# Performance work log

Hardware: AMD Instinct MI355X
Metric: run time of the kernel (lower is better)

The kernel has to match this reference:

```python
import jax, jax.numpy as jnp
import numpy as np

DIM = 256
H_GLOBAL = 8
H_LOCAL = 4  # max(1, num_heads // 2)
WINDOW = 5
HALF = WINDOW // 2
B, S = 4, 2048
EPS = 1e-5


def layer_norm(x, g, b):
    mu = jnp.mean(x, axis=-1, keepdims=True)
    var = jnp.mean(jnp.square(x - mu), axis=-1, keepdims=True)
    return (x - mu) * jax.lax.rsqrt(var + EPS) * g + b


def qkv_proj(x, in_w, in_b):
    qkv = x @ in_w.T + in_b
    return jnp.split(qkv, 3, axis=-1)


def global_mha(x, in_w, in_b, out_w, out_b, nh):
    Bq, Sq, D = x.shape
    hd = D // nh
    q, k, v = qkv_proj(x, in_w, in_b)
    q = q.reshape(Bq, Sq, nh, hd)
    k = k.reshape(Bq, Sq, nh, hd)
    v = v.reshape(Bq, Sq, nh, hd)
    scores = jnp.einsum('bqhd,bkhd->bhqk', q, k) / np.sqrt(hd).astype(np.float32)
    attn = jax.nn.softmax(scores, axis=-1)
    o = jnp.einsum('bhqk,bkhd->bqhd', attn, v).reshape(Bq, Sq, D)
    return o @ out_w.T + out_b


def local_mha(x, in_w, in_b, out_w, out_b, nh):
    # banded sliding-window attention, window = 2*HALF+1, per-query softmax
    Bq, Sq, D = x.shape
    hd = D // nh
    q, k, v = qkv_proj(x, in_w, in_b)
    kp = jnp.pad(k, ((0, 0), (HALF, HALF), (0, 0)))
    vp = jnp.pad(v, ((0, 0), (HALF, HALF), (0, 0)))
    # [B, S, W, D] windows of keys/values around each query position
    k_win = jnp.stack([kp[:, j:j + Sq] for j in range(WINDOW)], axis=2)
    v_win = jnp.stack([vp[:, j:j + Sq] for j in range(WINDOW)], axis=2)
    q = q.reshape(Bq, Sq, nh, hd)
    k_win = k_win.reshape(Bq, Sq, WINDOW, nh, hd)
    v_win = v_win.reshape(Bq, Sq, WINDOW, nh, hd)
    scores = jnp.einsum('bshd,bswhd->bshw', q, k_win) / np.sqrt(hd).astype(np.float32)
    idx = jnp.arange(Sq)[:, None] + jnp.arange(-HALF, HALF + 1)[None, :]  # [S, W]
    valid = (idx >= 0) & (idx < Sq)
    scores = jnp.where(valid[None, :, None, :], scores, -jnp.inf)
    attn = jax.nn.softmax(scores, axis=-1)
    o = jnp.einsum('bshw,bswhd->bshd', attn, v_win).reshape(Bq, Sq, D)
    return o @ out_w.T + out_b


def setup_inputs() -> dict:
    key = jax.random.key(0)
    ks = jax.random.split(key, 8)
    sc = 0.02
    d = DIM
    return {
        'x': jax.random.normal(ks[0], (B, S, d), jnp.float32),
        'g_in_w': jax.random.normal(ks[1], (3 * d, d), jnp.float32) * sc,
        'g_in_b': jnp.zeros((3 * d,), jnp.float32),
        'g_out_w': jax.random.normal(ks[2], (d, d), jnp.float32) * sc,
        'g_out_b': jnp.zeros((d,), jnp.float32),
        't_in_w': jax.random.normal(ks[3], (3 * d, d), jnp.float32) * sc,
        't_in_b': jnp.zeros((3 * d,), jnp.float32),
        't_out_w': jax.random.normal(ks[4], (d, d), jnp.float32) * sc,
        't_out_b': jnp.zeros((d,), jnp.float32),
        'fus_w1': jax.random.normal(ks[5], (2 * d, 2 * d), jnp.float32) * sc,
        'fus_b1': jnp.zeros((2 * d,), jnp.float32),
        'fus_w2': jax.random.normal(ks[6], (d, 2 * d), jnp.float32) * sc,
        'fus_b2': jnp.zeros((d,), jnp.float32),
        'ffn_w1': jax.random.normal(ks[7], (2 * d, d), jnp.float32) * sc,
        'ffn_b1': jnp.zeros((2 * d,), jnp.float32),
        'ffn_w2': jax.random.normal(jax.random.fold_in(key, 9), (d, 2 * d), jnp.float32) * sc,
        'ffn_b2': jnp.zeros((d,), jnp.float32),
        'gn_g': jnp.ones((d,), jnp.float32),
        'gn_b': jnp.zeros((d,), jnp.float32),
        'fn_g': jnp.ones((d,), jnp.float32),
        'fn_b': jnp.zeros((d,), jnp.float32),
    }


def reference(x, g_in_w, g_in_b, g_out_w, g_out_b,
              t_in_w, t_in_b, t_out_w, t_out_b,
              fus_w1, fus_b1, fus_w2, fus_b2,
              ffn_w1, ffn_b1, ffn_w2, ffn_b2,
              gn_g, gn_b, fn_g, fn_b):
    x_global = global_mha(x, g_in_w, g_in_b, g_out_w, g_out_b, H_GLOBAL)
    x_local = local_mha(x, t_in_w, t_in_b, t_out_w, t_out_b, H_LOCAL)
    x_comb = jnp.concatenate([x_global, x_local], axis=-1)
    x_fused = jax.nn.silu(x_comb @ fus_w1.T + fus_b1) @ fus_w2.T + fus_b2
    x = layer_norm(x + x_fused, gn_g, gn_b)
    x_ffn = jax.nn.silu(x @ ffn_w1.T + ffn_b1) @ ffn_w2.T + ffn_b2
    x = layer_norm(x + x_ffn, fn_g, fn_b)
    return x
```

## Files before the change

### kernel.cpp

```cpp
#include <hip/hip_runtime.h>

constexpr int Bb = 4;
constexpr int Ss = 2048;
constexpr int QSTR = 1536;

typedef __bf16 bf16x8 __attribute__((ext_vector_type(8)));
typedef __bf16 bf16x4 __attribute__((ext_vector_type(4)));
typedef float  f32x4  __attribute__((ext_vector_type(4)));

__device__ __forceinline__ void glds16(const void* g, void* l) {
    __builtin_amdgcn_global_load_lds(
        (const __attribute__((address_space(1))) unsigned int*)g,
        (__attribute__((address_space(3))) unsigned int*)l, 16, 0, 0);
}

struct CvtArgs {
    const float* src[9];
    __bf16* dst[9];
    int start[10];
};

__global__ __launch_bounds__(256) void convert_all(CvtArgs a)
{
    int e = 0;
    const int bid = blockIdx.x;
#pragma unroll
    for (int i = 0; i < 8; i++) if (bid >= a.start[i + 1]) e = i + 1;
    const int idx = (bid - a.start[e]) * 256 + threadIdx.x;
    const float* s = a.src[e];
    float4 v0 = *(const float4*)&s[(size_t)idx * 8];
    float4 v1 = *(const float4*)&s[(size_t)idx * 8 + 4];
    bf16x8 o;
    o[0] = (__bf16)v0.x; o[1] = (__bf16)v0.y; o[2] = (__bf16)v0.z; o[3] = (__bf16)v0.w;
    o[4] = (__bf16)v1.x; o[5] = (__bf16)v1.y; o[6] = (__bf16)v1.z; o[7] = (__bf16)v1.w;
    *(bf16x8*)&a.dst[e][(size_t)idx * 8] = o;
}

__global__ __launch_bounds__(256) void gemm128(
    const __bf16* __restrict__ A, const __bf16* __restrict__ W,
    const float* __restrict__ bias, const float* __restrict__ bias2, int bsplit,
    __bf16* __restrict__ C, int K, int ldc)
{
    __shared__ __bf16 As[128 * 64];
    __shared__ __bf16 Ws[128 * 64];
    const int tid = threadIdx.x;
    const int lane = tid & 63;
    const int wv = tid >> 6;
    const int wm = (wv >> 1) * 64;
    const int wn = (wv & 1) * 64;
    const int qrow = lane & 15;
    const int quad = lane >> 4;
    const int n0 = blockIdx.x * 128;
    const int m0 = blockIdx.y * 128;

    f32x4 acc[4][4];
#pragma unroll
    for (int i = 0; i < 4; i++)
#pragma unroll
        for (int j = 0; j < 4; j++) acc[i][j] = {0.f, 0.f, 0.f, 0.f};

    for (int k0 = 0; k0 < K; k0 += 64) {
        __syncthreads();
#pragma unroll
        for (int i = 0; i < 4; i++) {
            const int c = (wv * 4 + i) * 64 + lane;
            const int row = c >> 3, g = c & 7;
            const int gs = (g ^ (row & 7)) * 8;
            glds16(&A[(size_t)(m0 + row) * K + k0 + gs], &As[(wv * 4 + i) * 512]);
            glds16(&W[(size_t)(n0 + row) * K + k0 + gs], &Ws[(wv * 4 + i) * 512]);
        }
        __syncthreads();
#pragma unroll
        for (int ksub = 0; ksub < 2; ksub++) {
            const int gl = ksub * 4 + quad;
            bf16x8 af[4], bf[4];
#pragma unroll
            for (int mi = 0; mi < 4; mi++) {
                const int row = wm + mi * 16 + qrow;
                af[mi] = *(const bf16x8*)&As[row * 64 + (gl ^ (row & 7)) * 8];
            }
#pragma unroll
            for (int ni = 0; ni < 4; ni++) {
                const int row = wn + ni * 16 + qrow;
                bf[ni] = *(const bf16x8*)&Ws[row * 64 + (gl ^ (row & 7)) * 8];
            }
#pragma unroll
            for (int mi = 0; mi < 4; mi++)
#pragma unroll
                for (int ni = 0; ni < 4; ni++)
                    acc[mi][ni] = __builtin_amdgcn_mfma_f32_16x16x32_bf16(
                        af[mi], bf[ni], acc[mi][ni], 0, 0, 0);
        }
    }

    float bz[4];
#pragma unroll
    for (int ni = 0; ni < 4; ni++) {
        const int n = n0 + wn + ni * 16 + qrow;
        bz[ni] = (n < bsplit) ? bias[n] : bias2[n - bsplit];
    }
#pragma unroll
    for (int mi = 0; mi < 4; mi++)
#pragma unroll
        for (int r = 0; r < 4; r++) {
            const int row = m0 + wm + mi * 16 + quad * 4 + r;
#pragma unroll
            for (int ni = 0; ni < 4; ni++) {
                float v = acc[mi][ni][r] + bz[ni];
                C[(size_t)row * ldc + n0 + wn + ni * 16 + qrow] = (__bf16)v;
            }
        }
}

template<bool SILU, bool OUT_BF16>
__global__ __launch_bounds__(256) void gemm_small(
    const __bf16* __restrict__ A0, const __bf16* __restrict__ W0,
    const float* __restrict__ bias0, const __bf16* __restrict__ W1,
    const float* __restrict__ bias1, int nsplit, int aoff1, int coff1,
    void* __restrict__ C, int lda, int K, int ldc)
{
    __shared__ __bf16 As[32 * 128];
    __shared__ __bf16 Ws[64 * 128];
    const int tid = threadIdx.x;
    const int lane = tid & 63;
    const int wv = tid >> 6;
    const int wm = (wv >> 1) * 16;
    const int wn = (wv & 1) * 32;
    const int qrow = lane & 15;
    const int quad = lane >> 4;
    const bool second = (int)blockIdx.x >= nsplit;
    const int bx = second ? (blockIdx.x - nsplit) : blockIdx.x;
    const __bf16* A = second ? (A0 + aoff1) : A0;
    const __bf16* W = second ? W1 : W0;
    const float* bias = second ? bias1 : bias0;
    const int coff = second ? coff1 : 0;
    const int n0 = bx * 64;
    const int m0 = blockIdx.y * 32;

    f32x4 acc[2];
    acc[0] = {0.f, 0.f, 0.f, 0.f};
    acc[1] = {0.f, 0.f, 0.f, 0.f};

    for (int k0 = 0; k0 < K; k0 += 128) {
        __syncthreads();
#pragma unroll
        for (int i = 0; i < 2; i++) {
            const int c = (wv * 2 + i) * 64 + lane;
            const int row = c >> 4, s = c & 15;
            const int gs = ((s & 8) | ((s ^ row) & 7)) * 8;
            glds16(&A[(size_t)(m0 + row) * lda + k0 + gs], &As[(wv * 2 + i) * 512]);
        }
#pragma unroll
        for (int i = 0; i < 4; i++) {
            const int c = (wv * 4 + i) * 64 + lane;
            const int row = c >> 4, s = c & 15;
            const int gs = ((s & 8) | ((s ^ row) & 7)) * 8;
            glds16(&W[(size_t)(n0 + row) * K + k0 + gs], &Ws[(wv * 4 + i) * 512]);
        }
        __syncthreads();
#pragma unroll
        for (int ksub = 0; ksub < 4; ksub++) {
            const int gl = ksub * 4 + quad;
            bf16x8 af, bf[2];
            {
                const int row = wm + qrow;
                const int s = (gl & 8) | ((gl ^ row) & 7);
                af = *(const bf16x8*)&As[row * 128 + s * 8];
            }
#pragma unroll
            for (int ni = 0; ni < 2; ni++) {
                const int row = wn + ni * 16 + qrow;
                const int s = (gl & 8) | ((gl ^ row) & 7);
                bf[ni] = *(const bf16x8*)&Ws[row * 128 + s * 8];
            }
#pragma unroll
            for (int ni = 0; ni < 2; ni++)
                acc[ni] = __builtin_amdgcn_mfma_f32_16x16x32_bf16(
                    af, bf[ni], acc[ni], 0, 0, 0);
        }
    }

    float bz[2];
#pragma unroll
    for (int ni = 0; ni < 2; ni++) bz[ni] = bias[n0 + wn + ni * 16 + qrow];

#pragma unroll
    for (int r = 0; r < 4; r++) {
        const int row = m0 + wm + quad * 4 + r;
#pragma unroll
        for (int ni = 0; ni < 2; ni++) {
            float v = acc[ni][r] + bz[ni];
            if (SILU) v = v / (1.f + __expf(-v));
            const int col = coff + n0 + wn + ni * 16 + qrow;
            if (OUT_BF16)
                ((__bf16*)C)[(size_t)row * ldc + col] = (__bf16)v;
            else
                ((float*)C)[(size_t)row * ldc + col] = v;
        }
    }
}

__global__ __launch_bounds__(512) void attn_fused(
    const __bf16* __restrict__ qkv, __bf16* __restrict__ Op,
    float* __restrict__ Lp, __bf16* __restrict__ acat)
{
    __shared__ __bf16 Kl[64 * 32];
    __shared__ __bf16 Vt[32 * 72];
    __shared__ __bf16 Pl[8][16 * 72];

    const int t = threadIdx.x;
    const int lane = t & 63;
    const int wv = t >> 6;

    if (blockIdx.x < 2048) {
        const int bid = blockIdx.x;
        const int sp = bid & 3;
        const int qc = (bid >> 2) & 15;
        const int h  = (bid >> 6) & 7;
        const int b  = bid >> 9;
        const int bS = b * Ss;
        const int q0 = qc * 128;

        const int qrow = lane & 15;
        const int quad = lane >> 4;
        const float cQ = 1.4426950408889634f * 0.17677669529663687f;

        bf16x8 qf;
        {
            bf16x8 qraw = *(const bf16x8*)(qkv +
                (size_t)(bS + q0 + wv * 16 + qrow) * QSTR + h * 32 + quad * 8);
#pragma unroll
            for (int i = 0; i < 8; i++) qf[i] = (__bf16)((float)qraw[i] * cQ);
        }
        bf16x8 ones;
#pragma unroll
        for (int i = 0; i < 8; i++) ones[i] = (__bf16)1.0f;

        f32x4 o0 = {0.f, 0.f, 0.f, 0.f};
        f32x4 o1 = {0.f, 0.f, 0.f, 0.f};
        f32x4 lac = {0.f, 0.f, 0.f, 0.f};
        const f32x4 z = {0.f, 0.f, 0.f, 0.f};

        const int kc_c = wv * 64 + lane;
        const int kkey = kc_c >> 2, kdg = kc_c & 3;
        const int vkey = t & 63, vq = t >> 6;

        for (int kc = sp * 8; kc < sp * 8 + 8; kc++) {
            __syncthreads();
            if (wv < 4)
                glds16(qkv + (size_t)(bS + kc * 64 + kkey) * QSTR + 256 + h * 32 + kdg * 8,
                       &Kl[wv * 512]);
            {
                const __bf16* src = qkv + (size_t)(bS + kc * 64 + vkey) * QSTR
                                    + 512 + h * 32 + vq * 4;
                bf16x4 v = *(const bf16x4*)src;
#pragma unroll
                for (int i = 0; i < 4; i++) Vt[(vq * 4 + i) * 72 + vkey] = v[i];
            }
            __syncthreads();

            f32x4 s[4];
#pragma unroll
            for (int kg = 0; kg < 4; kg++) {
                bf16x8 kf = *(const bf16x8*)&Kl[(kg * 16 + qrow) * 32 + quad * 8];
                s[kg] = __builtin_amdgcn_mfma_f32_16x16x32_bf16(kf, qf, z, 0, 0, 0);
            }
#pragma unroll
            for (int kg = 0; kg < 4; kg++) {
                bf16x4 pk;
                pk[0] = (__bf16)exp2f(s[kg][0]);
                pk[1] = (__bf16)exp2f(s[kg][1]);
                pk[2] = (__bf16)exp2f(s[kg][2]);
                pk[3] = (__bf16)exp2f(s[kg][3]);
                *(bf16x4*)&Pl[wv][qrow * 72 + kg * 16 + quad * 4] = pk;
            }
            bf16x8 pf0 = *(const bf16x8*)&Pl[wv][qrow * 72 + quad * 8];
            bf16x8 pf1 = *(const bf16x8*)&Pl[wv][qrow * 72 + 32 + quad * 8];
            bf16x8 vf00 = *(const bf16x8*)&Vt[qrow * 72 + quad * 8];
            bf16x8 vf01 = *(const bf16x8*)&Vt[qrow * 72 + 32 + quad * 8];
            bf16x8 vf10 = *(const bf16x8*)&Vt[(16 + qrow) * 72 + quad * 8];
            bf16x8 vf11 = *(const bf16x8*)&Vt[(16 + qrow) * 72 + 32 + quad * 8];
            o0 = __builtin_amdgcn_mfma_f32_16x16x32_bf16(vf00, pf0, o0, 0, 0, 0);
            o1 = __builtin_amdgcn_mfma_f32_16x16x32_bf16(vf10, pf0, o1, 0, 0, 0);
            lac = __builtin_amdgcn_mfma_f32_16x16x32_bf16(ones, pf0, lac, 0, 0, 0);
            o0 = __builtin_amdgcn_mfma_f32_16x16x32_bf16(vf01, pf1, o0, 0, 0, 0);
            o1 = __builtin_amdgcn_mfma_f32_16x16x32_bf16(vf11, pf1, o1, 0, 0, 0);
            lac = __builtin_amdgcn_mfma_f32_16x16x32_bf16(ones, pf1, lac, 0, 0, 0);
        }

        const int gid = (b * 8 + h) * 2048 + q0 + wv * 16 + qrow;
        __bf16* po = Op + (size_t)sp * 2097152 + (size_t)gid * 32;
        bf16x4 w0, w1;
#pragma unroll
        for (int r = 0; r < 4; r++) { w0[r] = (__bf16)o0[r]; w1[r] = (__bf16)o1[r]; }
        *(bf16x4*)&po[quad * 4]      = w0;
        *(bf16x4*)&po[16 + quad * 4] = w1;
        if (quad == 0) Lp[sp * 65536 + gid] = lac[0];
    } else {
        const int w = (blockIdx.x - 2048) * 8 + wv;
        const int b = w >> 13;
        const int rem = w & 8191;
        const int s = rem >> 2;
        const int h = rem & 3;

        const float q = (float)qkv[(size_t)(b * Ss + s) * QSTR + 768 + h * 64 + lane];
        float sc[5], vv[5];
#pragma unroll
        for (int j = 0; j < 5; j++) {
            int pos = s + j - 2;
            bool valid = (pos >= 0) && (pos < Ss);
            int cpos = valid ? pos : 0;
            const size_t rb = (size_t)(b * Ss + cpos) * QSTR;
            float kj = valid ? (float)qkv[rb + 1024 + h * 64 + lane] : 0.f;
            vv[j] = valid ? (float)qkv[rb + 1280 + h * 64 + lane] : 0.f;
            float p = q * kj;
#pragma unroll
            for (int off = 32; off > 0; off >>= 1) p += __shfl_xor(p, off, 64);
            sc[j] = valid ? p * 0.125f : -1e30f;
        }
        float m = sc[0];
#pragma unroll
        for (int j = 1; j < 5; j++) m = fmaxf(m, sc[j]);
        float l = 0.f, o = 0.f;
#pragma unroll
        for (int j = 0; j < 5; j++) {
            float p = __expf(sc[j] - m);
            l += p; o += p * vv[j];
        }
        acat[(size_t)(b * Ss + s) * 512 + 256 + h * 64 + lane] = (__bf16)(o / l);
    }
}

__global__ __launch_bounds__(256) void attn_combine(
    const __bf16* __restrict__ Op, const float* __restrict__ Lp,
    __bf16* __restrict__ acat)
{
    const int t = blockIdx.x * 256 + threadIdx.x;
    const int gid = t >> 3;
    const int dg = t & 7;
    const int b = gid >> 14;
    const int h = (gid >> 11) & 7;
    const int q = gid & 2047;

    const float li = 1.f / (Lp[gid] + Lp[65536 + gid] + Lp[131072 + gid] + Lp[196608 + gid]);
    const __bf16* base = Op + (size_t)gid * 32 + dg * 4;
    bf16x4 a0 = *(const bf16x4*)&base[0];
    bf16x4 a1 = *(const bf16x4*)&base[2097152];
    bf16x4 a2 = *(const bf16x4*)&base[4194304];
    bf16x4 a3 = *(const bf16x4*)&base[6291456];
    bf16x4 r;
#pragma unroll
    for (int i = 0; i < 4; i++)
        r[i] = (__bf16)(((float)a0[i] + (float)a1[i] + (float)a2[i] + (float)a3[i]) * li);
    *(bf16x4*)&acat[(size_t)(b * Ss + q) * 512 + h * 32 + dg * 4] = r;
}

__global__ __launch_bounds__(256) void ln_residual(
    const float* __restrict__ a, const __bf16* __restrict__ r,
    const float* __restrict__ g, const float* __restrict__ be,
    float* __restrict__ out, __bf16* __restrict__ ob)
{
    const int lane = threadIdx.x & 63;
    const int tok = blockIdx.x * 4 + (threadIdx.x >> 6);
    float4 xa = ((const float4*)a)[(size_t)tok * 64 + lane];
    bf16x4 xr = *(const bf16x4*)&r[(size_t)tok * 256 + lane * 4];
    float4 x;
    x.x = xa.x + (float)xr[0]; x.y = xa.y + (float)xr[1];
    x.z = xa.z + (float)xr[2]; x.w = xa.w + (float)xr[3];
    float sum = x.x + x.y + x.z + x.w;
#pragma unroll
    for (int off = 32; off > 0; off >>= 1) sum += __shfl_xor(sum, off, 64);
    float mu = sum * (1.f / 256.f);
    float4 c;
    c.x = x.x - mu; c.y = x.y - mu; c.z = x.z - mu; c.w = x.w - mu;
    float sq = c.x * c.x + c.y * c.y + c.z * c.z + c.w * c.w;
#pragma unroll
    for (int off = 32; off > 0; off >>= 1) sq += __shfl_xor(sq, off, 64);
    float rs = rsqrtf(sq * (1.f / 256.f) + 1e-5f);
    float4 gg = ((const float4*)g)[lane];
    float4 bb = ((const float4*)be)[lane];
    float4 o;
    o.x = c.x * rs * gg.x + bb.x; o.y = c.y * rs * gg.y + bb.y;
    o.z = c.z * rs * gg.z + bb.z; o.w = c.w * rs * gg.w + bb.w;
    ((float4*)out)[(size_t)tok * 64 + lane] = o;
    if (ob) {
        bf16x4 hh;
        hh[0] = (__bf16)o.x; hh[1] = (__bf16)o.y; hh[2] = (__bf16)o.z; hh[3] = (__bf16)o.w;
        *(bf16x4*)&ob[(size_t)tok * 256 + lane * 4] = hh;
    }
}

extern "C" void kernel_launch(void* const* d_in, const int* in_sizes, int n_in,
                              void* d_out, int out_size, void* d_ws, size_t ws_size,
                              hipStream_t stream)
{
    const float* x      = (const float*)d_in[0];
    const float* g_in_w = (const float*)d_in[1];
    const float* g_in_b = (const float*)d_in[2];
    const float* g_out_w= (const float*)d_in[3];
    const float* g_out_b= (const float*)d_in[4];
    const float* t_in_w = (const float*)d_in[5];
    const float* t_in_b = (const float*)d_in[6];
    const float* t_out_w= (const float*)d_in[7];
    const float* t_out_b= (const float*)d_in[8];
    const float* fus_w1 = (const float*)d_in[9];
    const float* fus_b1 = (const float*)d_in[10];
    const float* fus_w2 = (const float*)d_in[11];
    const float* fus_b2 = (const float*)d_in[12];
    const float* ffn_w1 = (const float*)d_in[13];
    const float* ffn_b1 = (const float*)d_in[14];
    const float* ffn_w2 = (const float*)d_in[15];
    const float* ffn_b2 = (const float*)d_in[16];
    const float* gn_g   = (const float*)d_in[17];
    const float* gn_b   = (const float*)d_in[18];
    const float* fn_g   = (const float*)d_in[19];
    const float* fn_b   = (const float*)d_in[20];
    float* out = (float*)d_out;
    float* ws  = (float*)d_ws;

    __bf16* xb     = (__bf16*)(ws);
    __bf16* wb     = (__bf16*)(ws + 1048576);
    __bf16* qkvgl  = (__bf16*)(ws + 1638400);
    __bf16* acat   = (__bf16*)(ws + 7929856);
    __bf16* fcomb  = (__bf16*)(ws + 10027008);
    __bf16* h1     = (__bf16*)(ws + 12124160);
    __bf16* xfb    = (__bf16*)(ws + 14221312);
    float*  x2     = ws + 16318464;
    __bf16* x2b    = (__bf16*)(ws + 18415616);
    __bf16* h2     = h1;
    __bf16* xffb   = xfb;
    __bf16* Op = (__bf16*)(ws + 10027008);
    float*  Lp = ws + 18415616;

    __bf16* w_gin  = wb;
    __bf16* w_gout = wb + 393216;
    __bf16* w_tout = wb + 458752;
    __bf16* w_f1   = wb + 524288;
    __bf16* w_f2   = wb + 786432;
    __bf16* w_n1   = wb + 917504;
    __bf16* w_n2   = wb + 1048576;

    CvtArgs ca;
    ca.src[0] = x;      ca.dst[0] = xb;
    ca.src[1] = g_in_w; ca.dst[1] = w_gin;
    ca.src[2] = t_in_w; ca.dst[2] = w_gin + 196608;
    ca.src[3] = g_out_w;ca.dst[3] = w_gout;
    ca.src[4] = t_out_w;ca.dst[4] = w_tout;
    ca.src[5] = fus_w1; ca.dst[5] = w_f1;
    ca.src[6] = fus_w2; ca.dst[6] = w_f2;
    ca.src[7] = ffn_w1; ca.dst[7] = w_n1;
    ca.src[8] = ffn_w2; ca.dst[8] = w_n2;
    int st[10] = {0, 1024, 1120, 1216, 1248, 1280, 1408, 1472, 1536, 1600};
    for (int i = 0; i < 10; i++) ca.start[i] = st[i];

    convert_all<<<dim3(1600), 256, 0, stream>>>(ca);

    gemm128<<<dim3(12, 64), 256, 0, stream>>>(
        xb, w_gin, g_in_b, t_in_b, 768, qkvgl, 256, QSTR);
    attn_fused<<<dim3(6144), 512, 0, stream>>>(qkvgl, Op, Lp, acat);
    attn_combine<<<dim3(2048), 256, 0, stream>>>(Op, Lp, acat);
    gemm_small<false, true><<<dim3(8, 256), 256, 0, stream>>>(
        acat, w_gout, g_out_b, w_tout, t_out_b, 4, 256, 256, fcomb, 512, 256, 512);
    gemm_small<true,  true><<<dim3(8, 256), 256, 0, stream>>>(
        fcomb, w_f1, fus_b1, w_f1, fus_b1, 1 << 30, 0, 0, h1, 512, 512, 512);
    gemm_small<false, true><<<dim3(4, 256), 256, 0, stream>>>(
        h1, w_f2, fus_b2, w_f2, fus_b2, 1 << 30, 0, 0, xfb, 512, 512, 256);
    ln_residual<<<dim3(2048), 256, 0, stream>>>(x, xfb, gn_g, gn_b, x2, x2b);
    gemm_small<true,  true><<<dim3(8, 256), 256, 0, stream>>>(
        x2b, w_n1, ffn_b1, w_n1, ffn_b1, 1 << 30, 0, 0, h2, 256, 256, 512);
    gemm_small<false, true><<<dim3(4, 256), 256, 0, stream>>>(
        h2, w_n2, ffn_b2, w_n2, ffn_b2, 1 << 30, 0, 0, xffb, 512, 512, 256);
    ln_residual<<<dim3(2048), 256, 0, stream>>>(x2, xffb, fn_g, fn_b, out, nullptr);
}
```

Before: 238.3 us.

## Fuse output GEMM with residual add and LayerNorm into one kernel

Adds a gemm_ln kernel in which each block computes a 32-row by full 256-column output tile, adds bias and the fp32 residual, and does the LayerNorm reduction across waves through shared memory. It replaces the two gemm_small + ln_residual pairs, so two launches go away and the bf16 intermediate is never written to or read back from global memory. The new grid has only 256 blocks, each loading the whole 256xK weight slice per k-step, so parallelism is lower and weight traffic is redundant across blocks. Variance is now computed as E[x^2]-mu^2 and the pre-norm sum stays in fp32 instead of passing through bf16, which slightly changes numerics.

```diff
diff --git a/kernel.cpp b/kernel.cpp
--- a/kernel.cpp
+++ b/kernel.cpp
@@ -200,6 +200,127 @@
     }
 }
 
+__global__ __launch_bounds__(256) void gemm_ln(
+    const __bf16* __restrict__ A, const __bf16* __restrict__ W,
+    const float* __restrict__ bias, const float* __restrict__ xres,
+    const float* __restrict__ g, const float* __restrict__ be,
+    float* __restrict__ out, __bf16* __restrict__ ob, int K)
+{
+    __shared__ __bf16 As[32 * 64];
+    __shared__ __bf16 Ws[256 * 64];
+    __shared__ float redS[4][32];
+    __shared__ float redQ[4][32];
+
+    const int tid = threadIdx.x;
+    const int lane = tid & 63;
+    const int wv = tid >> 6;
+    const int qrow = lane & 15;
+    const int quad = lane >> 4;
+    const int m0 = blockIdx.x * 32;
+
+    f32x4 acc[2][4];
+#pragma unroll
+    for (int mi = 0; mi < 2; mi++)
+#pragma unroll
+        for (int ni = 0; ni < 4; ni++) acc[mi][ni] = {0.f, 0.f, 0.f, 0.f};
+
+    for (int k0 = 0; k0 < K; k0 += 64) {
+        __syncthreads();
+        {
+            const int c = wv * 64 + lane;
+            const int row = c >> 3, gch = c & 7;
+            const int gs = (gch ^ (row & 7)) * 8;
+            glds16(&A[(size_t)(m0 + row) * K + k0 + gs], &As[wv * 512]);
+        }
+#pragma unroll
+        for (int i = 0; i < 8; i++) {
+            const int c = (wv * 8 + i) * 64 + lane;
+            const int row = c >> 3, gch = c & 7;
+            const int gs = (gch ^ (row & 7)) * 8;
+            glds16(&W[(size_t)row * K + k0 + gs], &Ws[(wv * 8 + i) * 512]);
+        }
+        __syncthreads();
+#pragma unroll
+        for (int ksub = 0; ksub < 2; ksub++) {
+            const int gl = ksub * 4 + quad;
+            bf16x8 af[2], bf[4];
+#pragma unroll
+            for (int mi = 0; mi < 2; mi++) {
+                const int row = mi * 16 + qrow;
+                af[mi] = *(const bf16x8*)&As[row * 64 + (gl ^ (row & 7)) * 8];
+            }
+#pragma unroll
+            for (int ni = 0; ni < 4; ni++) {
+                const int row = wv * 64 + ni * 16 + qrow;
+                bf[ni] = *(const bf16x8*)&Ws[row * 64 + (gl ^ (row & 7)) * 8];
+            }
+#pragma unroll
+            for (int mi = 0; mi < 2; mi++)
+#pragma unroll
+                for (int ni = 0; ni < 4; ni++)
+                    acc[mi][ni] = __builtin_amdgcn_mfma_f32_16x16x32_bf16(
+                        af[mi], bf[ni], acc[mi][ni], 0, 0, 0);
+        }
+    }
+
+    float bz[4];
+#pragma unroll
+    for (int ni = 0; ni < 4; ni++) bz[ni] = bias[wv * 64 + ni * 16 + qrow];
+
+#pragma unroll
+    for (int mi = 0; mi < 2; mi++) {
+#pragma unroll
+        for (int r = 0; r < 4; r++) {
+            const int row = m0 + mi * 16 + quad * 4 + r;
+            float s = 0.f, q = 0.f;
+#pragma unroll
+            for (int ni = 0; ni < 4; ni++) {
+                const int col = wv * 64 + ni * 16 + qrow;
+                float v = acc[mi][ni][r] + bz[ni] + xres[(size_t)row * 256 + col];
+                acc[mi][ni][r] = v;
+                s += v; q += v * v;
+            }
+#pragma unroll
+            for (int off = 1; off < 16; off <<= 1) {
+                s += __shfl_xor(s, off, 64);
+                q += __shfl_xor(q, off, 64);
+            }
+            if (qrow == 0) {
+                redS[wv][mi * 16 + quad * 4 + r] = s;
+                redQ[wv][mi * 16 + quad * 4 + r] = q;
+            }
+        }
+    }
+    __syncthreads();
+
+    float gg[4], bb[4];
+#pragma unroll
+    for (int ni = 0; ni < 4; ni++) {
+        const int col = wv * 64 + ni * 16 + qrow;
+        gg[ni] = g[col]; bb[ni] = be[col];
+    }
+#pragma unroll
+    for (int mi = 0; mi < 2; mi++) {
+#pragma unroll
+        for (int r = 0; r < 4; r++) {
+            const int rl = mi * 16 + quad * 4 + r;
+            const float S = redS[0][rl] + redS[1][rl] + redS[2][rl] + redS[3][rl];
+            const float Q = redQ[0][rl] + redQ[1][rl] + redQ[2][rl] + redQ[3][rl];
+            const float mu = S * (1.f / 256.f);
+            const float var = Q * (1.f / 256.f) - mu * mu;
+            const float rs = rsqrtf(var + 1e-5f);
+            const int row = m0 + rl;
+#pragma unroll
+            for (int ni = 0; ni < 4; ni++) {
+                const int col = wv * 64 + ni * 16 + qrow;
+                const float v = (acc[mi][ni][r] - mu) * rs * gg[ni] + bb[ni];
+                out[(size_t)row * 256 + col] = v;
+                if (ob) ob[(size_t)row * 256 + col] = (__bf16)v;
+            }
+        }
+    }
+}
+
 __global__ __launch_bounds__(512) void attn_fused(
     const __bf16* __restrict__ qkv, __bf16* __restrict__ Op,
     float* __restrict__ Lp, __bf16* __restrict__ acat)
@@ -353,41 +474,6 @@
     for (int i = 0; i < 4; i++)
         r[i] = (__bf16)(((float)a0[i] + (float)a1[i] + (float)a2[i] + (float)a3[i]) * li);
     *(bf16x4*)&acat[(size_t)(b * Ss + q) * 512 + h * 32 + dg * 4] = r;
-}
-
-__global__ __launch_bounds__(256) void ln_residual(
-    const float* __restrict__ a, const __bf16* __restrict__ r,
-    const float* __restrict__ g, const float* __restrict__ be,
-    float* __restrict__ out, __bf16* __restrict__ ob)
-{
-    const int lane = threadIdx.x & 63;
-    const int tok = blockIdx.x * 4 + (threadIdx.x >> 6);
-    float4 xa = ((const float4*)a)[(size_t)tok * 64 + lane];
-    bf16x4 xr = *(const bf16x4*)&r[(size_t)tok * 256 + lane * 4];
-    float4 x;
-    x.x = xa.x + (float)xr[0]; x.y = xa.y + (float)xr[1];
-    x.z = xa.z + (float)xr[2]; x.w = xa.w + (float)xr[3];
-    float sum = x.x + x.y + x.z + x.w;
-#pragma unroll
-    for (int off = 32; off > 0; off >>= 1) sum += __shfl_xor(sum, off, 64);
-    float mu = sum * (1.f / 256.f);
-    float4 c;
-    c.x = x.x - mu; c.y = x.y - mu; c.z = x.z - mu; c.w = x.w - mu;
-    float sq = c.x * c.x + c.y * c.y + c.z * c.z + c.w * c.w;
-#pragma unroll
-    for (int off = 32; off > 0; off >>= 1) sq += __shfl_xor(sq, off, 64);
-    float rs = rsqrtf(sq * (1.f / 256.f) + 1e-5f);
-    float4 gg = ((const float4*)g)[lane];
-    float4 bb = ((const float4*)be)[lane];
-    float4 o;
-    o.x = c.x * rs * gg.x + bb.x; o.y = c.y * rs * gg.y + bb.y;
-    o.z = c.z * rs * gg.z + bb.z; o.w = c.w * rs * gg.w + bb.w;
-    ((float4*)out)[(size_t)tok * 64 + lane] = o;
-    if (ob) {
-        bf16x4 hh;
-        hh[0] = (__bf16)o.x; hh[1] = (__bf16)o.y; hh[2] = (__bf16)o.z; hh[3] = (__bf16)o.w;
-        *(bf16x4*)&ob[(size_t)tok * 256 + lane * 4] = hh;
-    }
 }
 
 extern "C" void kernel_launch(void* const* d_in, const int* in_sizes, int n_in,
@@ -424,11 +510,9 @@
     __bf16* acat   = (__bf16*)(ws + 7929856);
     __bf16* fcomb  = (__bf16*)(ws + 10027008);
     __bf16* h1     = (__bf16*)(ws + 12124160);
-    __bf16* xfb    = (__bf16*)(ws + 14221312);
     float*  x2     = ws + 16318464;
     __bf16* x2b    = (__bf16*)(ws + 18415616);
     __bf16* h2     = h1;
-    __bf16* xffb   = xfb;
     __bf16* Op = (__bf16*)(ws + 10027008);
     float*  Lp = ws + 18415616;
 
@@ -463,12 +547,10 @@
         acat, w_gout, g_out_b, w_tout, t_out_b, 4, 256, 256, fcomb, 512, 256, 512);
     gemm_small<true,  true><<<dim3(8, 256), 256, 0, stream>>>(
         fcomb, w_f1, fus_b1, w_f1, fus_b1, 1 << 30, 0, 0, h1, 512, 512, 512);
-    gemm_small<false, true><<<dim3(4, 256), 256, 0, stream>>>(
-        h1, w_f2, fus_b2, w_f2, fus_b2, 1 << 30, 0, 0, xfb, 512, 512, 256);
-    ln_residual<<<dim3(2048), 256, 0, stream>>>(x, xfb, gn_g, gn_b, x2, x2b);
+    gemm_ln<<<dim3(256), 256, 0, stream>>>(
+        h1, w_f2, fus_b2, x, gn_g, gn_b, x2, x2b, 512);
     gemm_small<true,  true><<<dim3(8, 256), 256, 0, stream>>>(
         x2b, w_n1, ffn_b1, w_n1, ffn_b1, 1 << 30, 0, 0, h2, 256, 256, 512);
-    gemm_small<false, true><<<dim3(4, 256), 256, 0, stream>>>(
-        h2, w_n2, ffn_b2, w_n2, ffn_b2, 1 << 30, 0, 0, xffb, 512, 512, 256);
-    ln_residual<<<dim3(2048), 256, 0, stream>>>(x2, xffb, fn_g, fn_b, out, nullptr);
-}
+    gemm_ln<<<dim3(256), 256, 0, stream>>>(
+        h2, w_n2, ffn_b2, x2, fn_g, fn_b, out, nullptr, 512);
+}
```

Measured after the change: 250.5 us. 1.05x slower.

## Fold attention output projections into fusion first-layer weights

Applied to the files above, without the earlier changes.

Adds a small per-call kernel that multiplies the fusion layer's first weight matrix by the global and local attention output-projection weights, and folds their biases into one effective weight and bias. The separate out-projection GEMM and its intermediate buffer are removed, so the concatenated attention output feeds straight into the SiLU fusion GEMM. This drops one 8192x512x256 GEMM and a round trip through memory. In exchange it adds a naive fp32 weight-folding kernel that runs on every call, and rounding changes because the product is formed in fp32 and then cast to bf16.

```diff
diff --git a/kernel.cpp b/kernel.cpp
--- a/kernel.cpp
+++ b/kernel.cpp
@@ -34,6 +34,39 @@
     o[0] = (__bf16)v0.x; o[1] = (__bf16)v0.y; o[2] = (__bf16)v0.z; o[3] = (__bf16)v0.w;
     o[4] = (__bf16)v1.x; o[5] = (__bf16)v1.y; o[6] = (__bf16)v1.z; o[7] = (__bf16)v1.w;
     *(bf16x8*)&a.dst[e][(size_t)idx * 8] = o;
+}
+
+__global__ __launch_bounds__(256) void wfold(
+    const float* __restrict__ w_f1, const float* __restrict__ g_out_w,
+    const float* __restrict__ t_out_w, const float* __restrict__ g_out_b,
+    const float* __restrict__ t_out_b, const float* __restrict__ f_b1,
+    __bf16* __restrict__ Weff, float* __restrict__ beff)
+{
+    const int i0 = blockIdx.x * 4;
+    const int j = threadIdx.x;
+    float accg[4] = {0.f, 0.f, 0.f, 0.f};
+    float acct[4] = {0.f, 0.f, 0.f, 0.f};
+    float accb[4] = {0.f, 0.f, 0.f, 0.f};
+    for (int k = 0; k < 256; k++) {
+        const float gw = g_out_w[k * 256 + j];
+        const float tw = t_out_w[k * 256 + j];
+        const float gb = g_out_b[k];
+        const float tb = t_out_b[k];
+#pragma unroll
+        for (int r = 0; r < 4; r++) {
+            const float ag = w_f1[(size_t)(i0 + r) * 512 + k];
+            const float at = w_f1[(size_t)(i0 + r) * 512 + 256 + k];
+            accg[r] += ag * gw;
+            acct[r] += at * tw;
+            accb[r] += ag * gb + at * tb;
+        }
+    }
+#pragma unroll
+    for (int r = 0; r < 4; r++) {
+        Weff[(size_t)(i0 + r) * 512 + j]       = (__bf16)accg[r];
+        Weff[(size_t)(i0 + r) * 512 + 256 + j] = (__bf16)acct[r];
+        if (j == 0) beff[i0 + r] = f_b1[i0 + r] + accb[r];
+    }
 }
 
 __global__ __launch_bounds__(256) void gemm128(
@@ -114,9 +147,8 @@
 
 template<bool SILU, bool OUT_BF16>
 __global__ __launch_bounds__(256) void gemm_small(
-    const __bf16* __restrict__ A0, const __bf16* __restrict__ W0,
-    const float* __restrict__ bias0, const __bf16* __restrict__ W1,
-    const float* __restrict__ bias1, int nsplit, int aoff1, int coff1,
+    const __bf16* __restrict__ A, const __bf16* __restrict__ W,
+    const float* __restrict__ bias,
     void* __restrict__ C, int lda, int K, int ldc)
 {
     __shared__ __bf16 As[32 * 128];
@@ -128,13 +160,7 @@
     const int wn = (wv & 1) * 32;
     const int qrow = lane & 15;
     const int quad = lane >> 4;
-    const bool second = (int)blockIdx.x >= nsplit;
-    const int bx = second ? (blockIdx.x - nsplit) : blockIdx.x;
-    const __bf16* A = second ? (A0 + aoff1) : A0;
-    const __bf16* W = second ? W1 : W0;
-    const float* bias = second ? bias1 : bias0;
-    const int coff = second ? coff1 : 0;
-    const int n0 = bx * 64;
+    const int n0 = blockIdx.x * 64;
     const int m0 = blockIdx.y * 32;
 
     f32x4 acc[2];
@@ -191,7 +217,7 @@
         for (int ni = 0; ni < 2; ni++) {
             float v = acc[ni][r] + bz[ni];
             if (SILU) v = v / (1.f + __expf(-v));
-            const int col = coff + n0 + wn + ni * 16 + qrow;
+            const int col = n0 + wn + ni * 16 + qrow;
             if (OUT_BF16)
                 ((__bf16*)C)[(size_t)row * ldc + col] = (__bf16)v;
             else
@@ -422,9 +448,10 @@
     __bf16* wb     = (__bf16*)(ws + 1048576);
     __bf16* qkvgl  = (__bf16*)(ws + 1638400);
     __bf16* acat   = (__bf16*)(ws + 7929856);
-    __bf16* fcomb  = (__bf16*)(ws + 10027008);
     __bf16* h1     = (__bf16*)(ws + 12124160);
     __bf16* xfb    = (__bf16*)(ws + 14221312);
+    __bf16* Weff   = (__bf16*)(ws + 15269888);
+    float*  beff   = ws + 15335424;
     float*  x2     = ws + 16318464;
     __bf16* x2b    = (__bf16*)(ws + 18415616);
     __bf16* h2     = h1;
@@ -433,9 +460,6 @@
     float*  Lp = ws + 18415616;
 
     __bf16* w_gin  = wb;
-    __bf16* w_gout = wb + 393216;
-    __bf16* w_tout = wb + 458752;
-    __bf16* w_f1   = wb + 524288;
     __bf16* w_f2   = wb + 786432;
     __bf16* w_n1   = wb + 917504;
     __bf16* w_n2   = wb + 1048576;
@@ -444,9 +468,9 @@
     ca.src[0] = x;      ca.dst[0] = xb;
     ca.src[1] = g_in_w; ca.dst[1] = w_gin;
     ca.src[2] = t_in_w; ca.dst[2] = w_gin + 196608;
-    ca.src[3] = g_out_w;ca.dst[3] = w_gout;
-    ca.src[4] = t_out_w;ca.dst[4] = w_tout;
-    ca.src[5] = fus_w1; ca.dst[5] = w_f1;
+    ca.src[3] = g_out_w;ca.dst[3] = wb + 393216;
+    ca.src[4] = t_out_w;ca.dst[4] = wb + 458752;
+    ca.src[5] = fus_w1; ca.dst[5] = wb + 524288;
     ca.src[6] = fus_w2; ca.dst[6] = w_f2;
     ca.src[7] = ffn_w1; ca.dst[7] = w_n1;
     ca.src[8] = ffn_w2; ca.dst[8] = w_n2;
@@ -454,21 +478,21 @@
     for (int i = 0; i < 10; i++) ca.start[i] = st[i];
 
     convert_all<<<dim3(1600), 256, 0, stream>>>(ca);
+    wfold<<<dim3(128), 256, 0, stream>>>(
+        fus_w1, g_out_w, t_out_w, g_out_b, t_out_b, fus_b1, Weff, beff);
 
     gemm128<<<dim3(12, 64), 256, 0, stream>>>(
         xb, w_gin, g_in_b, t_in_b, 768, qkvgl, 256, QSTR);
     attn_fused<<<dim3(6144), 512, 0, stream>>>(qkvgl, Op, Lp, acat);
     attn_combine<<<dim3(2048), 256, 0, stream>>>(Op, Lp, acat);
-    gemm_small<false, true><<<dim3(8, 256), 256, 0, stream>>>(
-        acat, w_gout, g_out_b, w_tout, t_out_b, 4, 256, 256, fcomb, 512, 256, 512);
     gemm_small<true,  true><<<dim3(8, 256), 256, 0, stream>>>(
-        fcomb, w_f1, fus_b1, w_f1, fus_b1, 1 << 30, 0, 0, h1, 512, 512, 512);
+        acat, Weff, beff, h1, 512, 512, 512);
     gemm_small<false, true><<<dim3(4, 256), 256, 0, stream>>>(
-        h1, w_f2, fus_b2, w_f2, fus_b2, 1 << 30, 0, 0, xfb, 512, 512, 256);
+        h1, w_f2, fus_b2, xfb, 512, 512, 256);
     ln_residual<<<dim3(2048), 256, 0, stream>>>(x, xfb, gn_g, gn_b, x2, x2b);
     gemm_small<true,  true><<<dim3(8, 256), 256, 0, stream>>>(
-        x2b, w_n1, ffn_b1, w_n1, ffn_b1, 1 << 30, 0, 0, h2, 256, 256, 512);
+        x2b, w_n1, ffn_b1, h2, 256, 256, 512);
     gemm_small<false, true><<<dim3(4, 256), 256, 0, stream>>>(
-        h2, w_n2, ffn_b2, w_n2, ffn_b2, 1 << 30, 0, 0, xffb, 512, 512, 256);
+        h2, w_n2, ffn_b2, xffb, 512, 512, 256);
     ln_residual<<<dim3(2048), 256, 0, stream>>>(x2, xffb, fn_g, fn_b, out, nullptr);
 }
```

Measured after the change: 255.0 us. +7.0%, slower.
